# Kernel optimization log

Hardware: AMD Instinct MI355X
Metric: run time of the kernel (lower is better)

Reference implementation:

```python
import jax, jax.numpy as jnp
import numpy as np

MIN_FP16 = float(np.finfo(np.float16).min)  # -65504.0, matches torch.finfo(torch.float16).min


def _apply_rotary(x, cos, sin):
    # x: [B, H, S, D]; cos/sin: [S, D//2]
    # Equivalent to view_as_complex on interleaved pairs, multiply by freq_cis, view_as_real.
    xr = x[..., 0::2]
    xi = x[..., 1::2]
    c = cos[None, None]  # [1,1,S,D//2]
    s = sin[None, None]
    out_r = xr * c - xi * s
    out_i = xr * s + xi * c
    return jnp.stack([out_r, out_i], axis=-1).reshape(x.shape)


def setup_inputs() -> dict:
    key = jax.random.key(0)
    ks = jax.random.split(key, 4)
    B, S, D_MODEL, H = 2, 2048, 1024, 16
    HS = D_MODEL // H  # 64
    x = jax.random.normal(ks[0], (B, S, D_MODEL), dtype=jnp.float32)
    # Standard RoPE frequencies: theta_i = 10000^(-2i/HS)
    inv_freq = 1.0 / (10000.0 ** (np.arange(0, HS, 2, dtype=np.float32) / HS))  # [HS//2]
    t = np.arange(S, dtype=np.float32)
    angles = np.outer(t, inv_freq)  # [S, HS//2]
    cos = jnp.asarray(np.cos(angles))
    sin = jnp.asarray(np.sin(angles))
    mask = jnp.tril(jnp.ones((S, S), dtype=jnp.int32))[None, None]  # [1,1,S,S] causal
    scale = 1.0 / np.sqrt(D_MODEL)
    W_proj = jax.random.normal(ks[1], (D_MODEL, 3 * D_MODEL), dtype=jnp.float32) * scale
    b_proj = jnp.zeros((3 * D_MODEL,), dtype=jnp.float32)
    W_ff = jax.random.normal(ks[2], (D_MODEL, D_MODEL), dtype=jnp.float32) * scale
    b_ff = jnp.zeros((D_MODEL,), dtype=jnp.float32)
    return {"x": x, "cos_q": cos, "sin_q": sin, "cos_k": cos, "sin_k": sin,
            "mask": mask, "W_proj": W_proj, "b_proj": b_proj, "W_ff": W_ff, "b_ff": b_ff}


def reference(x, cos_q, sin_q, cos_k, sin_k, mask, W_proj, b_proj, W_ff, b_ff):
    B, S, d_model = x.shape
    H = 16
    HS = d_model // H
    head_scale = jnp.sqrt(jnp.float32(HS))

    # fused QKV projection, then split: [B,S,3*dm] -> [3,B,H,S,HS]
    x_proj = x @ W_proj + b_proj
    x_proj = x_proj.reshape(B, S, 3, H, HS).transpose(2, 0, 3, 1, 4)
    q, k, v = x_proj[0], x_proj[1], x_proj[2]

    # mask path: cache pre-RoPE k,v
    next_prefix_kv = jnp.stack([k, v])  # [2,B,H,S,HS]

    q = _apply_rotary(q, cos_q, sin_q)
    k = _apply_rotary(k, cos_k, sin_k)

    scores = jnp.einsum('bhqd,bhkd->bhqk', q, k) / head_scale
    scores = jnp.where(mask == 0, jnp.float32(MIN_FP16), scores)
    probs = jax.nn.softmax(scores, axis=-1)
    attn_o = jnp.einsum('bhqk,bhkd->bhqd', probs, v)  # [B,H,S,HS]

    attn_o = attn_o.transpose(0, 2, 1, 3).reshape(B, S, d_model)
    ff_o = attn_o @ W_ff + b_ff
    return ff_o, next_prefix_kv
```

## Files before the change

### kernel.cpp

```cpp
#include <hip/hip_runtime.h>
#include <stdint.h>

#define DM    1024
#define NH    16
#define HS    64
#define S_LEN 2048

typedef short bf16x8 __attribute__((ext_vector_type(8)));
typedef float f32x4  __attribute__((ext_vector_type(4)));
typedef unsigned short u16x4 __attribute__((ext_vector_type(4)));

__device__ __forceinline__ uint16_t f2b(float f) {
    union { float f; uint32_t i; } x; x.f = f;
    uint32_t r = x.i + 0x7fffu + ((x.i >> 16) & 1u);
    return (uint16_t)(r >> 16);
}
__device__ __forceinline__ uint32_t pack2(float a, float b) {
    return (uint32_t)f2b(a) | ((uint32_t)f2b(b) << 16);
}
__device__ __forceinline__ f32x4 mfma16(bf16x8 a, bf16x8 b, f32x4 c) {
    return __builtin_amdgcn_mfma_f32_16x16x32_bf16(a, b, c, 0, 0, 0);
}
template<int CTRL>
__device__ __forceinline__ float dpp_max(float x) {
    union { float f; int i; } u; u.f = x;
    int y = __builtin_amdgcn_update_dpp(u.i, u.i, CTRL, 0xF, 0xF, true);
    union { int i; float f; } v; v.i = y;
    return fmaxf(x, v.f);
}

__global__ __launch_bounds__(256) void convert_bf16(
    const float* __restrict__ in, uint16_t* __restrict__ out)
{
    const size_t i = (size_t)blockIdx.x * 256 + threadIdx.x;
    const float4* p = (const float4*)in + i * 2;
    float4 a = p[0], b = p[1];
    uint4 o;
    o.x = pack2(a.x, a.y); o.y = pack2(a.z, a.w);
    o.z = pack2(b.x, b.y); o.w = pack2(b.z, b.w);
    ((uint4*)out)[i] = o;
}

__global__ __launch_bounds__(256) void transpose_w(
    const float* __restrict__ W, uint16_t* __restrict__ WT, int N)
{
    __shared__ float T[32][33];
    const int tx = threadIdx.x & 31, ty = threadIdx.x >> 5;
    const int n0 = blockIdx.x * 32, k0 = blockIdx.y * 32;
    #pragma unroll
    for (int i = 0; i < 4; ++i)
        T[ty + i * 8][tx] = W[(size_t)(k0 + ty + i * 8) * N + n0 + tx];
    __syncthreads();
    #pragma unroll
    for (int i = 0; i < 4; ++i)
        WT[(size_t)(n0 + ty + i * 8) * 1024 + k0 + tx] = f2b(T[tx][ty + i * 8]);
}

#define LOADK(K0, A0_, A1_, B0_, B1_)                                                      \
    do {                                                                                   \
        if (ABF) {                                                                         \
            const uint16_t* ap_ = (const uint16_t*)Araw + (size_t)(m0 + sm) * 1024 + (K0) + skc; \
            A0_ = *(const uint4*)ap_;                                                      \
            A1_ = *(const uint4*)(ap_ + 8);                                                \
        } else {                                                                           \
            const float* ap_ = (const float*)Araw + (size_t)(m0 + sm) * 1024 + (K0) + skc; \
            float4 f0_ = *(const float4*)(ap_ + 0),  f1_ = *(const float4*)(ap_ + 4);      \
            float4 f2_ = *(const float4*)(ap_ + 8),  f3_ = *(const float4*)(ap_ + 12);     \
            A0_.x = pack2(f0_.x, f0_.y); A0_.y = pack2(f0_.z, f0_.w);                      \
            A0_.z = pack2(f1_.x, f1_.y); A0_.w = pack2(f1_.z, f1_.w);                      \
            A1_.x = pack2(f2_.x, f2_.y); A1_.y = pack2(f2_.z, f2_.w);                      \
            A1_.z = pack2(f3_.x, f3_.y); A1_.w = pack2(f3_.z, f3_.w);                      \
        }                                                                                  \
        const uint16_t* bp_ = BT + (size_t)(n0 + sm) * 1024 + (K0) + skc;                  \
        B0_ = *(const uint4*)bp_;                                                          \
        B1_ = *(const uint4*)(bp_ + 8);                                                    \
    } while (0)

#define STOREK(BUF, A0_, A1_, B0_, B1_)                                                    \
    do {                                                                                   \
        *(uint4*)&As[BUF][sm][skc]     = A0_;                                              \
        *(uint4*)&As[BUF][sm][skc + 8] = A1_;                                              \
        *(uint4*)&Bs[BUF][sm][skc]     = B0_;                                              \
        *(uint4*)&Bs[BUF][sm][skc + 8] = B1_;                                              \
    } while (0)

#define COMPUTEK(BUF)                                                                      \
    do {                                                                                   \
        bf16x8 af_[4], bf_[4];                                                             \
        _Pragma("unroll")                                                                  \
        for (int mi = 0; mi < 4; ++mi)                                                     \
            af_[mi] = *(const bf16x8*)&As[BUF][wm + mi * 16 + li][quad * 8];               \
        _Pragma("unroll")                                                                  \
        for (int ni = 0; ni < 4; ++ni)                                                     \
            bf_[ni] = *(const bf16x8*)&Bs[BUF][wn + ni * 16 + li][quad * 8];               \
        _Pragma("unroll")                                                                  \
        for (int mi = 0; mi < 4; ++mi)                                                     \
            _Pragma("unroll")                                                              \
            for (int ni = 0; ni < 4; ++ni)                                                 \
                acc[mi][ni] = mfma16(af_[mi], bf_[ni], acc[mi][ni]);                       \
    } while (0)

template<int MODE, bool ABF, bool WV>
__global__ __launch_bounds__(256) void gemm_mfma(
    const void* __restrict__ Araw,
    const uint16_t* __restrict__ BT,
    const float* __restrict__ bias,
    int N,
    const float* __restrict__ cq, const float* __restrict__ sq,
    const float* __restrict__ ck, const float* __restrict__ sk,
    uint16_t* __restrict__ qbuf, uint16_t* __restrict__ kbuf,
    float* __restrict__ kout, float* __restrict__ vout,
    uint16_t* __restrict__ vtb,
    float* __restrict__ Cout)
{
    __shared__ uint16_t As[2][128][40];
    __shared__ uint16_t Bs[2][128][40];

    const int tid  = threadIdx.x;
    const int wave = tid >> 6, lane = tid & 63;
    const int quad = lane >> 4, li = lane & 15;
    const int wm = (wave >> 1) * 64, wn = (wave & 1) * 64;
    const int m0 = blockIdx.y * 128, n0 = blockIdx.x * 128;

    f32x4 acc[4][4];
    #pragma unroll
    for (int a = 0; a < 4; ++a)
        #pragma unroll
        for (int c = 0; c < 4; ++c)
            acc[a][c] = (f32x4){0.f, 0.f, 0.f, 0.f};

    const int sm = tid >> 1, skc = (tid & 1) * 16;

    uint4 Aa0, Aa1, Ba0, Ba1;
    uint4 Ab0, Ab1, Bb0, Bb1;

    LOADK(0, Aa0, Aa1, Ba0, Ba1);
    STOREK(0, Aa0, Aa1, Ba0, Ba1);
    LOADK(32, Ab0, Ab1, Bb0, Bb1);
    __syncthreads();

    for (int t = 0; t < 16; ++t) {
        const int kb = t * 64;
        if (t < 15) LOADK(kb + 64, Aa0, Aa1, Ba0, Ba1);
        COMPUTEK(0);
        STOREK(1, Ab0, Ab1, Bb0, Bb1);
        __syncthreads();
        if (t < 15) LOADK(kb + 96, Ab0, Ab1, Bb0, Bb1);
        COMPUTEK(1);
        if (t < 15) {
            STOREK(0, Aa0, Aa1, Ba0, Ba1);
            __syncthreads();
        }
    }

    if (MODE == 1) {
        #pragma unroll
        for (int ni = 0; ni < 4; ++ni) {
            const int n = n0 + wn + ni * 16 + li;
            const float bb = bias[n];
            #pragma unroll
            for (int mi = 0; mi < 4; ++mi)
                #pragma unroll
                for (int r = 0; r < 4; ++r) {
                    const int m = m0 + wm + mi * 16 + quad * 4 + r;
                    Cout[(size_t)m * N + n] = acc[mi][ni][r] + bb;
                }
        }
    } else {
        #pragma unroll
        for (int ni = 0; ni < 4; ++ni) {
            const int n   = n0 + wn + ni * 16 + li;
            const int sel = n >> 10;
            const int d   = n & 1023;
            const int h   = d >> 6;
            const int hd  = d & 63;
            const int i0  = hd >> 1;
            const float bb = bias[n];
            #pragma unroll
            for (int mi = 0; mi < 4; ++mi) {
                const int mb = m0 + wm + mi * 16 + quad * 4;
                const int b  = mb >> 11;
                const int s0 = mb & 2047;
                float vv[4];
                #pragma unroll
                for (int r = 0; r < 4; ++r) {
                    const int s = s0 + r;
                    const float val  = acc[mi][ni][r] + bb;
                    const float part = __shfl_xor(val, 1);
                    const size_t idx = ((size_t)(b * NH + h) * S_LEN + s) * HS + hd;
                    if (sel == 0) {
                        float c = cq[s * 32 + i0], sn = sq[s * 32 + i0];
                        float o = (hd & 1) ? (part * sn + val * c) : (val * c - part * sn);
                        qbuf[idx] = f2b(o * 0.125f);
                    } else if (sel == 1) {
                        kout[idx] = val;
                        float c = ck[s * 32 + i0], sn = sk[s * 32 + i0];
                        float o = (hd & 1) ? (part * sn + val * c) : (val * c - part * sn);
                        kbuf[idx] = f2b(o);
                    } else {
                        vout[idx] = val;
                        vv[r] = val;
                    }
                }
                if (WV && sel == 2) {
                    u16x4 u;
                    u[0] = f2b(vv[0]); u[1] = f2b(vv[1]);
                    u[2] = f2b(vv[2]); u[3] = f2b(vv[3]);
                    *(u16x4*)&vtb[((size_t)(b * NH + h) * HS + hd) * S_LEN + s0] = u;
                }
            }
        }
    }
}

__global__ __launch_bounds__(256) void attn_mfma(
    const uint16_t* __restrict__ qbuf,
    const uint16_t* __restrict__ kbuf,
    const uint16_t* __restrict__ vtb,
    uint16_t* __restrict__ obuf)
{
    __shared__ uint16_t Ks[64][72];
    __shared__ uint16_t Vt[64][72];
    __shared__ uint16_t Ps[64][68];

    const int i  = blockIdx.x;
    const int bh = i >> 5;
    const int jj = i & 31;
    const int g  = jj >> 3, cc = jj & 7;
    const int qt = (g == 0) ? (31 - cc) : (g == 1) ? cc : (g == 2) ? (23 - cc) : (8 + cc);
    const int h = bh & 15, b = bh >> 4;
    const int tid = threadIdx.x;
    const int wave = tid >> 6, lane = tid & 63;
    const int quad = lane >> 4, li = lane & 15;
    const int wrow0 = wave * 16;

    const short onebf = (short)0x3F80;
    const bf16x8 kOnes = {onebf, onebf, onebf, onebf, onebf, onebf, onebf, onebf};

    const uint16_t* qp = qbuf + ((size_t)bh * S_LEN + qt * 64 + wrow0 + li) * HS + quad * 8;
    const bf16x8 aq0 = *(const bf16x8*)qp;
    const bf16x8 aq1 = *(const bf16x8*)(qp + 32);

    f32x4 oacc[4];
    float m_i[4], l_i[4];
    #pragma unroll
    for (int r = 0; r < 4; ++r) {
        m_i[r] = -1e30f; l_i[r] = 0.f;
        oacc[r] = (f32x4){0.f, 0.f, 0.f, 0.f};
    }

    const int row = tid >> 2, c = (tid & 3) * 16;
    uint4 kr0, kr1, vr0, vr1;

    auto load_kv = [&](int kt) {
        const uint16_t* kp = kbuf + ((size_t)bh * S_LEN + kt * 64 + row) * HS + c;
        kr0 = *(const uint4*)kp;
        kr1 = *(const uint4*)(kp + 8);
        const uint16_t* vp = vtb + ((size_t)bh * HS + row) * S_LEN + kt * 64 + c;
        vr0 = *(const uint4*)vp;
        vr1 = *(const uint4*)(vp + 8);
    };
    load_kv(0);

    for (int kt = 0; kt <= qt; ++kt) {
        __syncthreads();
        *(uint4*)&Ks[row][c]     = kr0;
        *(uint4*)&Ks[row][c + 8] = kr1;
        *(uint4*)&Vt[row][c]     = vr0;
        *(uint4*)&Vt[row][c + 8] = vr1;
        __syncthreads();
        if (kt < qt) load_kv(kt + 1);

        f32x4 sacc[4];
        __builtin_amdgcn_s_setprio(1);
        #pragma unroll
        for (int ni = 0; ni < 4; ++ni) {
            bf16x8 b0 = *(const bf16x8*)&Ks[ni * 16 + li][quad * 8];
            bf16x8 b1 = *(const bf16x8*)&Ks[ni * 16 + li][32 + quad * 8];
            f32x4 z = (f32x4){0.f, 0.f, 0.f, 0.f};
            z = mfma16(aq0, b0, z);
            sacc[ni] = mfma16(aq1, b1, z);
        }
        __builtin_amdgcn_s_setprio(0);

        const bool diag = (kt == qt);
        float p[4][4];
        #pragma unroll
        for (int ni = 0; ni < 4; ++ni)
            #pragma unroll
            for (int r = 0; r < 4; ++r) {
                float v = sacc[ni][r];
                if (diag && (ni * 16 + li > wrow0 + quad * 4 + r)) v = -65504.f;
                p[ni][r] = v;
            }
        float alp[4];
        #pragma unroll
        for (int r = 0; r < 4; ++r) {
            float mx = fmaxf(fmaxf(p[0][r], p[1][r]), fmaxf(p[2][r], p[3][r]));
            mx = dpp_max<0xB1>(mx);
            mx = dpp_max<0x4E>(mx);
            mx = dpp_max<0x124>(mx);
            mx = dpp_max<0x128>(mx);
            float mnew  = fmaxf(m_i[r], mx);
            alp[r] = __expf(m_i[r] - mnew);
            m_i[r] = mnew;
            #pragma unroll
            for (int ni = 0; ni < 4; ++ni)
                p[ni][r] = __expf(p[ni][r] - mnew);
            #pragma unroll
            for (int ni = 0; ni < 4; ++ni) oacc[ni][r] *= alp[r];
        }

        #pragma unroll
        for (int ni = 0; ni < 4; ++ni)
            #pragma unroll
            for (int r = 0; r < 4; ++r)
                Ps[wrow0 + quad * 4 + r][ni * 16 + li] = f2b(p[ni][r]);

        bf16x8 pa0 = *(const bf16x8*)&Ps[wrow0 + li][quad * 8];
        bf16x8 pa1 = *(const bf16x8*)&Ps[wrow0 + li][32 + quad * 8];

        __builtin_amdgcn_s_setprio(1);
        f32x4 ls = (f32x4){0.f, 0.f, 0.f, 0.f};
        ls = mfma16(pa0, kOnes, ls);
        ls = mfma16(pa1, kOnes, ls);

        #pragma unroll
        for (int ni = 0; ni < 4; ++ni) {
            bf16x8 v0 = *(const bf16x8*)&Vt[ni * 16 + li][quad * 8];
            bf16x8 v1 = *(const bf16x8*)&Vt[ni * 16 + li][32 + quad * 8];
            oacc[ni] = mfma16(pa0, v0, oacc[ni]);
            oacc[ni] = mfma16(pa1, v1, oacc[ni]);
        }
        __builtin_amdgcn_s_setprio(0);

        #pragma unroll
        for (int r = 0; r < 4; ++r)
            l_i[r] = l_i[r] * alp[r] + ls[r];
    }

    #pragma unroll
    for (int ni = 0; ni < 4; ++ni)
        #pragma unroll
        for (int r = 0; r < 4; ++r) {
            const int qg = qt * 64 + wrow0 + quad * 4 + r;
            obuf[((size_t)b * S_LEN + qg) * DM + h * HS + ni * 16 + li] =
                f2b(oacc[ni][r] / l_i[r]);
        }
}

extern "C" void kernel_launch(void* const* d_in, const int* in_sizes, int n_in,
                              void* d_out, int out_size, void* d_ws, size_t ws_size,
                              hipStream_t stream) {
    const float* x  = (const float*)d_in[0];
    const float* cq = (const float*)d_in[1];
    const float* sq = (const float*)d_in[2];
    const float* ck = (const float*)d_in[3];
    const float* sk = (const float*)d_in[4];
    const float* Wp = (const float*)d_in[6];
    const float* bp = (const float*)d_in[7];
    const float* Wf = (const float*)d_in[8];
    const float* bf = (const float*)d_in[9];

    float* out  = (float*)d_out;
    float* ffo  = out;
    float* kout = out + 4194304;
    float* vout = out + 8388608;

    uint16_t* qbuf = (uint16_t*)d_ws;
    uint16_t* kbuf = qbuf + 4194304;
    uint16_t* abuf = kbuf + 4194304;
    uint16_t* vtb  = abuf + 4194304;
    uint16_t* xbf  = vtb  + 4194304;
    uint16_t* WpT  = abuf;
    uint16_t* WfT  = qbuf;

    const bool has_xbf = ws_size >= (size_t)40 * 1024 * 1024;

    dim3 blk(256);
    transpose_w<<<dim3(96, 32), blk, 0, stream>>>(Wp, WpT, 3072);
    if (has_xbf) {
        convert_bf16<<<dim3(2048), blk, 0, stream>>>(x, xbf);
        gemm_mfma<0, true, true><<<dim3(24, 32), blk, 0, stream>>>(
            xbf, WpT, bp, 3072, cq, sq, ck, sk,
            qbuf, kbuf, kout, vout, vtb, nullptr);
    } else {
        gemm_mfma<0, false, true><<<dim3(24, 32), blk, 0, stream>>>(
            x, WpT, bp, 3072, cq, sq, ck, sk,
            qbuf, kbuf, kout, vout, vtb, nullptr);
    }
    attn_mfma<<<dim3(1024), blk, 0, stream>>>(qbuf, kbuf, vtb, abuf);
    transpose_w<<<dim3(32, 32), blk, 0, stream>>>(Wf, WfT, 1024);
    gemm_mfma<1, true, false><<<dim3(8, 32), blk, 0, stream>>>(
        abuf, WfT, bf, 1024, nullptr, nullptr, nullptr, nullptr,
        nullptr, nullptr, nullptr, nullptr, nullptr, ffo);
}
```

Measured before the change: 291.9 us.

## Stage bf16 GEMM tiles via global_load_lds and use exp2 softmax

For bf16 A inputs, the GEMM now copies tiles straight from global memory into LDS with global_load_lds instead of loading into registers and storing them. The LDS row padding is removed to fit the direct-copy layout, and the k-loop runs as a 32-step double buffer. Separately, the log2(e) factor is folded into the Q scale so softmax can use the hardware exp2 instead of __expf. Dropping the padding may bring back LDS bank conflicts on the fragment reads. The masked fill value is still -65504 in the scaled domain, which does not change the result here.

```diff
diff --git a/kernel.cpp b/kernel.cpp
--- a/kernel.cpp
+++ b/kernel.cpp
@@ -20,6 +20,9 @@
 }
 __device__ __forceinline__ f32x4 mfma16(bf16x8 a, bf16x8 b, f32x4 c) {
     return __builtin_amdgcn_mfma_f32_16x16x32_bf16(a, b, c, 0, 0, 0);
+}
+__device__ __forceinline__ float fast_exp2(float x) {
+    return __builtin_amdgcn_exp2f(x);
 }
 template<int CTRL>
 __device__ __forceinline__ float dpp_max(float x) {
@@ -100,6 +103,26 @@
                 acc[mi][ni] = mfma16(af_[mi], bf_[ni], acc[mi][ni]);                       \
     } while (0)
 
+#define STAGE_GLL(BUF, K0)                                                                 \
+    do {                                                                                   \
+        const uint16_t* ga_ = (const uint16_t*)Araw +                                      \
+            (size_t)(m0 + wave * 32 + (lane >> 2)) * 1024 + (K0) + (lane & 3) * 8;         \
+        __builtin_amdgcn_global_load_lds(                                                  \
+            (const __attribute__((address_space(1))) void*)ga_,                            \
+            (__attribute__((address_space(3))) void*)&As[BUF][wave * 32][0], 16, 0, 0);    \
+        __builtin_amdgcn_global_load_lds(                                                  \
+            (const __attribute__((address_space(1))) void*)(ga_ + 16 * 1024),              \
+            (__attribute__((address_space(3))) void*)&As[BUF][wave * 32 + 16][0], 16, 0, 0);\
+        const uint16_t* gb_ = BT +                                                         \
+            (size_t)(n0 + wave * 32 + (lane >> 2)) * 1024 + (K0) + (lane & 3) * 8;         \
+        __builtin_amdgcn_global_load_lds(                                                  \
+            (const __attribute__((address_space(1))) void*)gb_,                            \
+            (__attribute__((address_space(3))) void*)&Bs[BUF][wave * 32][0], 16, 0, 0);    \
+        __builtin_amdgcn_global_load_lds(                                                  \
+            (const __attribute__((address_space(1))) void*)(gb_ + 16 * 1024),              \
+            (__attribute__((address_space(3))) void*)&Bs[BUF][wave * 32 + 16][0], 16, 0, 0);\
+    } while (0)
+
 template<int MODE, bool ABF, bool WV>
 __global__ __launch_bounds__(256) void gemm_mfma(
     const void* __restrict__ Araw,
@@ -113,8 +136,8 @@
     uint16_t* __restrict__ vtb,
     float* __restrict__ Cout)
 {
-    __shared__ uint16_t As[2][128][40];
-    __shared__ uint16_t Bs[2][128][40];
+    __shared__ uint16_t As[2][128][32];
+    __shared__ uint16_t Bs[2][128][32];
 
     const int tid  = threadIdx.x;
     const int wave = tid >> 6, lane = tid & 63;
@@ -131,25 +154,36 @@
 
     const int sm = tid >> 1, skc = (tid & 1) * 16;
 
-    uint4 Aa0, Aa1, Ba0, Ba1;
-    uint4 Ab0, Ab1, Bb0, Bb1;
-
-    LOADK(0, Aa0, Aa1, Ba0, Ba1);
-    STOREK(0, Aa0, Aa1, Ba0, Ba1);
-    LOADK(32, Ab0, Ab1, Bb0, Bb1);
-    __syncthreads();
-
-    for (int t = 0; t < 16; ++t) {
-        const int kb = t * 64;
-        if (t < 15) LOADK(kb + 64, Aa0, Aa1, Ba0, Ba1);
-        COMPUTEK(0);
-        STOREK(1, Ab0, Ab1, Bb0, Bb1);
+    if constexpr (ABF) {
+        STAGE_GLL(0, 0);
         __syncthreads();
-        if (t < 15) LOADK(kb + 96, Ab0, Ab1, Bb0, Bb1);
-        COMPUTEK(1);
-        if (t < 15) {
-            STOREK(0, Aa0, Aa1, Ba0, Ba1);
+        for (int t = 0; t < 32; t += 2) {
+            if (t + 1 < 32) STAGE_GLL(1, (t + 1) * 32);
+            COMPUTEK(0);
             __syncthreads();
+            if (t + 2 < 32) STAGE_GLL(0, (t + 2) * 32);
+            COMPUTEK(1);
+            __syncthreads();
+        }
+    } else {
+        uint4 Aa0, Aa1, Ba0, Ba1;
+        uint4 Ab0, Ab1, Bb0, Bb1;
+        LOADK(0, Aa0, Aa1, Ba0, Ba1);
+        STOREK(0, Aa0, Aa1, Ba0, Ba1);
+        LOADK(32, Ab0, Ab1, Bb0, Bb1);
+        __syncthreads();
+        for (int t = 0; t < 16; ++t) {
+            const int kb = t * 64;
+            if (t < 15) LOADK(kb + 64, Aa0, Aa1, Ba0, Ba1);
+            COMPUTEK(0);
+            STOREK(1, Ab0, Ab1, Bb0, Bb1);
+            __syncthreads();
+            if (t < 15) LOADK(kb + 96, Ab0, Ab1, Bb0, Bb1);
+            COMPUTEK(1);
+            if (t < 15) {
+                STOREK(0, Aa0, Aa1, Ba0, Ba1);
+                __syncthreads();
+            }
         }
     }
 
@@ -191,7 +225,7 @@
                     if (sel == 0) {
                         float c = cq[s * 32 + i0], sn = sq[s * 32 + i0];
                         float o = (hd & 1) ? (part * sn + val * c) : (val * c - part * sn);
-                        qbuf[idx] = f2b(o * 0.125f);
+                        qbuf[idx] = f2b(o * 0.18033688f);
                     } else if (sel == 1) {
                         kout[idx] = val;
                         float c = ck[s * 32 + i0], sn = sk[s * 32 + i0];
@@ -302,11 +336,11 @@
             mx = dpp_max<0x124>(mx);
             mx = dpp_max<0x128>(mx);
             float mnew  = fmaxf(m_i[r], mx);
-            alp[r] = __expf(m_i[r] - mnew);
+            alp[r] = fast_exp2(m_i[r] - mnew);
             m_i[r] = mnew;
             #pragma unroll
             for (int ni = 0; ni < 4; ++ni)
-                p[ni][r] = __expf(p[ni][r] - mnew);
+                p[ni][r] = fast_exp2(p[ni][r] - mnew);
             #pragma unroll
             for (int ni = 0; ni < 4; ++ni) oacc[ni][r] *= alp[r];
         }
```

Result: no change. 294.3 us (+0.8%).
